# Kernel tuning notes

Hardware: AMD Instinct MI355X
Metric: run time of the kernel (lower is better)

The kernel has to match this reference:

```python
import jax, jax.numpy as jnp
import numpy as np

C = 256
CR = 32  # C // nc_reduce

def setup_inputs() -> dict:
    key = jax.random.key(0)
    ks = jax.random.split(key, 8)
    B, H, W = 4, 64, 64
    x = jax.random.normal(ks[0], (B, C, H, W), dtype=jnp.float32)
    s_in = 1.0 / np.sqrt(C)
    Wq = jax.random.uniform(ks[1], (CR, C), jnp.float32, -s_in, s_in)
    bq = jax.random.uniform(ks[2], (CR,), jnp.float32, -s_in, s_in)
    Wk = jax.random.uniform(ks[3], (CR, C), jnp.float32, -s_in, s_in)
    bk = jax.random.uniform(ks[4], (CR,), jnp.float32, -s_in, s_in)
    Wv = jax.random.uniform(ks[5], (C, C), jnp.float32, -s_in, s_in)
    bv = jax.random.uniform(ks[6], (C,), jnp.float32, -s_in, s_in)
    gamma = jnp.zeros((1,), dtype=jnp.float32)
    return {"x": x, "Wq": Wq, "bq": bq, "Wk": Wk, "bk": bk,
            "Wv": Wv, "bv": bv, "gamma": gamma}

def reference(x, Wq, bq, Wk, bk, Wv, bv, gamma):
    B, Cc, H, W = x.shape
    N = H * W
    xf = x.reshape(B, Cc, N)                       # [B, C, N]
    # 1x1 convs == per-position channel projections
    q = jnp.einsum('dc,bcn->bdn', Wq, xf) + bq[None, :, None]  # [B, CR, N]
    k = jnp.einsum('dc,bcn->bdn', Wk, xf) + bk[None, :, None]  # [B, CR, N]
    v = jnp.einsum('dc,bcn->bdn', Wv, xf) + bv[None, :, None]  # [B, C, N]
    # energy[b,i,j] = q[:, :, i] . k[:, :, j]  (no scaling, as in source)
    energy = jnp.einsum('bdi,bdj->bij', q, k)      # [B, N, N]
    attn = jax.nn.softmax(energy, axis=-1)
    # out[b,c,i] = sum_j v[b,c,j] * attn[b,i,j]
    outv = jnp.einsum('bcj,bij->bci', v, attn)     # [B, C, N]
    out = gamma[0] * outv.reshape(B, Cc, H, W) + x
    return out
```

## Files before the change

### kernel.cpp

```cpp
#include <hip/hip_runtime.h>
#include <hip/hip_bf16.h>

#define NB 4
#define CCH 256
#define CRD 32
#define NN 4096

typedef __attribute__((ext_vector_type(8))) short short8;
typedef __attribute__((ext_vector_type(4))) float floatx4;
typedef __attribute__((ext_vector_type(4))) int intx4;
typedef __attribute__((ext_vector_type(2))) unsigned int uintx2;

__device__ __forceinline__ unsigned short f2bf(float f) {
  unsigned u = __builtin_bit_cast(unsigned, f);
  u += 0x7FFFu + ((u >> 16) & 1u);
  return (unsigned short)(u >> 16);
}

__device__ __forceinline__ unsigned short f2bf_c(float f) {
  f = fminf(fmaxf(f, -1.0e4f), 1.0e4f);
  unsigned u = __builtin_bit_cast(unsigned, f);
  u += 0x7FFFu + ((u >> 16) & 1u);
  return (unsigned short)(u >> 16);
}

__device__ __forceinline__ unsigned pack2c(float a, float b) {
  return (unsigned)f2bf_c(a) | ((unsigned)f2bf_c(b) << 16);
}

__device__ __forceinline__ float sat(float v) {
  return fminf(fmaxf(v, -1.0e30f), 1.0e30f);
}

__device__ __forceinline__ short8 ld_frag_g(const unsigned short* p) {
  return __builtin_bit_cast(short8, *(const intx4*)p);
}

__global__ __launch_bounds__(256) void gemm_qkv_fused(
    const float* __restrict__ x,
    const float* __restrict__ Wq, const float* __restrict__ bq,
    const float* __restrict__ Wk, const float* __restrict__ bk,
    const float* __restrict__ Wv, const float* __restrict__ bv,
    unsigned short* __restrict__ qT, unsigned short* __restrict__ kT,
    unsigned short* __restrict__ vv)
{
  __shared__ __align__(16) unsigned short xs[64 * 264];
  __shared__ __align__(16) unsigned short ws[64 * 264];

  const int tid  = threadIdx.x;
  const int wave = tid >> 6;
  const int lane = tid & 63;
  const int lq   = lane >> 4;
  const int lm   = lane & 15;
  const int n0   = blockIdx.x << 6;
  const int mg   = blockIdx.y;
  const int b    = blockIdx.z;

  {
    const int nn = lane;
    const int cg = wave;
    const float* xb = x + ((size_t)b << 20) + n0 + nn;
#pragma unroll
    for (int it = 0; it < 16; ++it) {
      const int c0 = it * 16 + cg * 4;
      const float v0 = xb[(size_t)(c0 + 0) << 12];
      const float v1 = xb[(size_t)(c0 + 1) << 12];
      const float v2 = xb[(size_t)(c0 + 2) << 12];
      const float v3 = xb[(size_t)(c0 + 3) << 12];
      uintx2 u;
      u[0] = pack2c(v0, v1);
      u[1] = pack2c(v2, v3);
      *(uintx2*)(xs + nn * 264 + c0) = u;
    }
  }

  const int mt_lo = mg ? 3 : 0;
  const int mt_hi = mg ? 5 : 3;

  for (int mt = mt_lo; mt < mt_hi; ++mt) {
#pragma unroll
    for (int i = 0; i < 16; ++i) {
      const int u  = i * 256 + tid;
      const int m  = u >> 6;
      const int o4 = (u & 63) * 4;
      const float* src = (mt == 0)
          ? (m < 32 ? Wq + (size_t)m * CCH : Wk + (size_t)(m - 32) * CCH)
          : Wv + (size_t)((mt - 1) * 64 + m) * CCH;
      const floatx4 f = *(const floatx4*)(src + o4);
      uintx2 uu;
      uu[0] = pack2c(f[0], f[1]);
      uu[1] = pack2c(f[2], f[3]);
      *(uintx2*)(ws + m * 264 + o4) = uu;
    }
    __syncthreads();

    floatx4 acc[4];
#pragma unroll
    for (int t = 0; t < 4; ++t) acc[t] = (floatx4){0.f, 0.f, 0.f, 0.f};

#pragma unroll
    for (int k0 = 0; k0 < 8; ++k0) {
      short8 af[4];
#pragma unroll
      for (int ms = 0; ms < 4; ++ms)
        af[ms] = __builtin_bit_cast(short8,
            *(const intx4*)(ws + (ms * 16 + lm) * 264 + k0 * 32 + lq * 8));
      const short8 bf = __builtin_bit_cast(short8,
          *(const intx4*)(xs + (wave * 16 + lm) * 264 + k0 * 32 + lq * 8));
#pragma unroll
      for (int ms = 0; ms < 4; ++ms)
        acc[ms] = __builtin_amdgcn_mfma_f32_16x16x32_bf16(af[ms], bf,
                                                          acc[ms], 0, 0, 0);
    }
    __syncthreads();

    if (mt == 0) {
      const int n = n0 + wave * 16 + lm;
#pragma unroll
      for (int ms = 0; ms < 4; ++ms) {
        const int d0 = (ms & 1) * 16 + lq * 4;
        const float* bias = (ms < 2) ? bq : bk;
        unsigned short* dst = (ms < 2) ? qT : kT;
        uintx2 u;
        u[0] = pack2c(acc[ms][0] + bias[d0],     acc[ms][1] + bias[d0 + 1]);
        u[1] = pack2c(acc[ms][2] + bias[d0 + 2], acc[ms][3] + bias[d0 + 3]);
        *(uintx2*)(dst + (size_t)(b * NN + n) * CRD + d0) = u;
      }
    } else {
      const int cb = (mt - 1) * 64;
      unsigned short* vb2 = ws;
#pragma unroll
      for (int ms = 0; ms < 4; ++ms)
#pragma unroll
        for (int r = 0; r < 4; ++r) {
          const int c = ms * 16 + lq * 4 + r;
          vb2[c * 64 + wave * 16 + lm] = f2bf_c(acc[ms][r] + bv[cb + c]);
        }
      __syncthreads();
#pragma unroll
      for (int it = 0; it < 2; ++it) {
        const int u = it * 256 + tid;
        const int m = u >> 3;
        const int o = (u & 7) * 8;
        *(intx4*)(vv + (size_t)(b * CCH + cb + m) * NN + n0 + o) =
            *(const intx4*)(vb2 + m * 64 + o);
      }
      __syncthreads();
    }
  }
}

__global__ __launch_bounds__(512) void attn_kernel(
    const float* __restrict__ x, const float* __restrict__ gamma_p,
    const unsigned short* __restrict__ qT, const unsigned short* __restrict__ kT,
    const unsigned short* __restrict__ vv, float* __restrict__ out)
{
  __shared__ __align__(16) unsigned char smem[65536 + 2 * 4 * 2176];

  const int tid  = threadIdx.x;
  const int wave = tid >> 6;
  const int wg   = wave >> 1;
  const int cs   = wave & 1;
  const int lane = tid & 63;
  const int lq   = lane >> 4;
  const int lm   = lane & 15;
  const int xcd = blockIdx.x & 7;
  const int pos = blockIdx.x >> 3;
  const int b   = xcd >> 1;
  const int i0  = (((xcd & 1) << 5) | pos) << 6;

  const unsigned short* kTb = kT + (size_t)b * NN * CRD;
  const unsigned short* vb  = vv + (size_t)b * CCH * NN;

  const short8 qf =
      ld_frag_g(qT + (size_t)(b * NN + i0 + wg * 16 + lm) * CRD + lq * 8);

  int vs_g[4];
  int vs_off[4];
#pragma unroll
  for (int m = 0; m < 4; ++m) {
    const int u  = m * 512 + tid;
    const int c  = u >> 3;
    const int jb = u & 7;
    vs_g[m]   = c * NN + jb * 8;
    vs_off[m] = c * 128 + ((jb ^ (c & 7)) * 16);
  }

  floatx4 acc[8];
#pragma unroll
  for (int t = 0; t < 8; ++t) acc[t] = (floatx4){0.f, 0.f, 0.f, 0.f};
  float lsum[4] = {0.f, 0.f, 0.f, 0.f};

  intx4 vreg[4];
#pragma unroll
  for (int m = 0; m < 4; ++m)
    vreg[m] = *(const intx4*)(vb + vs_g[m]);
  short8 kf[2];
#pragma unroll
  for (int jt = 0; jt < 2; ++jt)
    kf[jt] = ld_frag_g(kTb + (size_t)((cs * 2 + jt) * 16 + lm) * CRD + lq * 8);

  const floatx4 zf = {0.f, 0.f, 0.f, 0.f};

#pragma unroll 1
  for (int k = 0; k < 64; ++k) {
    unsigned char* vbuf = smem + ((k & 1) << 15);
    unsigned char* pb   = smem + 65536 + (k & 1) * 8704 + wg * 2176;

#pragma unroll
    for (int m = 0; m < 4; ++m)
      *(intx4*)(vbuf + vs_off[m]) = vreg[m];

    floatx4 S[2];
#pragma unroll
    for (int jt = 0; jt < 2; ++jt) {
      S[jt] = __builtin_amdgcn_mfma_f32_16x16x32_bf16(qf, kf[jt], zf, 0, 0, 0);
#pragma unroll
      for (int r = 0; r < 4; ++r) {
        const float p = __expf(fminf(fmaxf(S[jt][r], -40.f), 40.f));
        S[jt][r] = p;
        lsum[r] += p;
      }
    }
#pragma unroll
    for (int jt = 0; jt < 2; ++jt)
#pragma unroll
      for (int r = 0; r < 4; ++r)
        *(unsigned short*)(pb + (lq * 4 + r) * 136 +
                           (((cs * 2 + jt) * 16 + lm) << 1)) = f2bf(S[jt][r]);

    asm volatile("s_waitcnt lgkmcnt(0)" ::: "memory");
    __builtin_amdgcn_s_barrier();

    if (k < 63) {
      const int j0n = (k + 1) << 6;
#pragma unroll
      for (int m = 0; m < 4; ++m)
        vreg[m] = *(const intx4*)(vb + vs_g[m] + j0n);
#pragma unroll
      for (int jt = 0; jt < 2; ++jt)
        kf[jt] = ld_frag_g(kTb +
                           (size_t)(j0n + (cs * 2 + jt) * 16 + lm) * CRD + lq * 8);
    }

#pragma unroll
    for (int ks = 0; ks < 2; ++ks) {
      const unsigned char* pa = pb + lm * 136 + ks * 64 + lq * 16;
      struct U128 { unsigned long long a, b; } pp;
      pp.a = *(const unsigned long long*)pa;
      pp.b = *(const unsigned long long*)(pa + 8);
      const short8 pf = __builtin_bit_cast(short8, pp);
#pragma unroll
      for (int nt = 0; nt < 8; ++nt) {
        const int c = cs * 128 + nt * 16 + lm;
        const short8 vf = __builtin_bit_cast(
            short8,
            *(const intx4*)(smem + ((k & 1) << 15) + c * 128 +
                            (((ks * 4 + lq) ^ (lm & 7)) * 16)));
        acc[nt] = __builtin_amdgcn_mfma_f32_16x16x32_bf16(pf, vf, acc[nt], 0, 0, 0);
      }
    }
    (void)vbuf;
  }

  __syncthreads();
  floatx4 lv;
#pragma unroll
  for (int r = 0; r < 4; ++r) lv[r] = lsum[r];
  *(floatx4*)(smem + ((wave * 64 + lane) << 4)) = lv;
  __syncthreads();
  const floatx4 lpart = *(const floatx4*)(smem + (((wave ^ 1) * 64 + lane) << 4));

  float inv[4];
#pragma unroll
  for (int r = 0; r < 4; ++r) {
    float v = lsum[r] + lpart[r];
    v += __shfl_xor(v, 1);
    v += __shfl_xor(v, 2);
    v += __shfl_xor(v, 4);
    v += __shfl_xor(v, 8);
    inv[r] = 1.0f / v;
  }

  const float gm = gamma_p[0];
#pragma unroll
  for (int nt = 0; nt < 8; ++nt) {
#pragma unroll
    for (int r = 0; r < 4; ++r) {
      const int c = cs * 128 + nt * 16 + lm;
      const int i = i0 + wg * 16 + lq * 4 + r;
      const size_t idx = (size_t)(b * CCH + c) * NN + i;
      out[idx] = gm * sat(acc[nt][r] * inv[r]) + x[idx];
    }
  }
}

extern "C" void kernel_launch(void* const* d_in, const int* in_sizes, int n_in,
                              void* d_out, int out_size, void* d_ws, size_t ws_size,
                              hipStream_t stream) {
  (void)in_sizes; (void)n_in; (void)out_size; (void)ws_size;
  const float* x     = (const float*)d_in[0];
  const float* Wq    = (const float*)d_in[1];
  const float* bq    = (const float*)d_in[2];
  const float* Wk    = (const float*)d_in[3];
  const float* bk    = (const float*)d_in[4];
  const float* Wv    = (const float*)d_in[5];
  const float* bv    = (const float*)d_in[6];
  const float* gamma = (const float*)d_in[7];

  unsigned short* qT = (unsigned short*)d_ws;
  unsigned short* kT = qT + (size_t)NB * NN * CRD;
  unsigned short* vv = kT + (size_t)NB * NN * CRD;

  gemm_qkv_fused<<<dim3(64, 2, 4), 256, 0, stream>>>(x, Wq, bq, Wk, bk, Wv, bv,
                                                     qT, kT, vv);
  attn_kernel<<<dim3(256, 1, 1), 512, 0, stream>>>(x, gamma, qT, kT, vv,
                                                   (float*)d_out);
}
```

Baseline: 166.3 us.

## Software-pipeline attention loop so next tile's scores overlap current PV MFMAs

```diff
diff --git a/kernel.cpp b/kernel.cpp
--- a/kernel.cpp
+++ b/kernel.cpp
@@ -191,6 +191,8 @@
   for (int t = 0; t < 8; ++t) acc[t] = (floatx4){0.f, 0.f, 0.f, 0.f};
   float lsum[4] = {0.f, 0.f, 0.f, 0.f};
 
+  const floatx4 zf = {0.f, 0.f, 0.f, 0.f};
+
   intx4 vreg[4];
 #pragma unroll
   for (int m = 0; m < 4; ++m)
@@ -200,52 +202,73 @@
   for (int jt = 0; jt < 2; ++jt)
     kf[jt] = ld_frag_g(kTb + (size_t)((cs * 2 + jt) * 16 + lm) * CRD + lq * 8);
 
-  const floatx4 zf = {0.f, 0.f, 0.f, 0.f};
+#pragma unroll
+  for (int m = 0; m < 4; ++m)
+    *(intx4*)(smem + vs_off[m]) = vreg[m];
+  {
+    unsigned char* pb0 = smem + 65536 + wg * 2176;
+#pragma unroll
+    for (int jt = 0; jt < 2; ++jt) {
+      const floatx4 S = __builtin_amdgcn_mfma_f32_16x16x32_bf16(
+          qf, kf[jt], zf, 0, 0, 0);
+#pragma unroll
+      for (int r = 0; r < 4; ++r) {
+        const float p = __expf(fminf(fmaxf(S[r], -40.f), 40.f));
+        lsum[r] += p;
+        *(unsigned short*)(pb0 + (lq * 4 + r) * 136 +
+                           (((cs * 2 + jt) * 16 + lm) << 1)) = f2bf(p);
+      }
+    }
+  }
+#pragma unroll
+  for (int m = 0; m < 4; ++m)
+    vreg[m] = *(const intx4*)(vb + vs_g[m] + 64);
+#pragma unroll
+  for (int jt = 0; jt < 2; ++jt)
+    kf[jt] = ld_frag_g(kTb + (size_t)(64 + (cs * 2 + jt) * 16 + lm) * CRD +
+                       lq * 8);
 
 #pragma unroll 1
-  for (int k = 0; k < 64; ++k) {
-    unsigned char* vbuf = smem + ((k & 1) << 15);
-    unsigned char* pb   = smem + 65536 + (k & 1) * 8704 + wg * 2176;
-
-#pragma unroll
-    for (int m = 0; m < 4; ++m)
-      *(intx4*)(vbuf + vs_off[m]) = vreg[m];
-
-    floatx4 S[2];
-#pragma unroll
-    for (int jt = 0; jt < 2; ++jt) {
-      S[jt] = __builtin_amdgcn_mfma_f32_16x16x32_bf16(qf, kf[jt], zf, 0, 0, 0);
-#pragma unroll
-      for (int r = 0; r < 4; ++r) {
-        const float p = __expf(fminf(fmaxf(S[jt][r], -40.f), 40.f));
-        S[jt][r] = p;
-        lsum[r] += p;
-      }
-    }
-#pragma unroll
-    for (int jt = 0; jt < 2; ++jt)
-#pragma unroll
-      for (int r = 0; r < 4; ++r)
-        *(unsigned short*)(pb + (lq * 4 + r) * 136 +
-                           (((cs * 2 + jt) * 16 + lm) << 1)) = f2bf(S[jt][r]);
-
+  for (int k = 0; k < 63; ++k) {
     asm volatile("s_waitcnt lgkmcnt(0)" ::: "memory");
     __builtin_amdgcn_s_barrier();
 
-    if (k < 63) {
-      const int j0n = (k + 1) << 6;
+    unsigned char* vbp = smem + ((k & 1) << 15);
+    unsigned char* pbp = smem + 65536 + (k & 1) * 8704 + wg * 2176;
+    unsigned char* vbn = smem + (((k + 1) & 1) << 15);
+    unsigned char* pbn = smem + 65536 + ((k + 1) & 1) * 8704 + wg * 2176;
+
+#pragma unroll
+    for (int m = 0; m < 4; ++m)
+      *(intx4*)(vbn + vs_off[m]) = vreg[m];
+
+#pragma unroll
+    for (int jt = 0; jt < 2; ++jt) {
+      const floatx4 S = __builtin_amdgcn_mfma_f32_16x16x32_bf16(
+          qf, kf[jt], zf, 0, 0, 0);
+#pragma unroll
+      for (int r = 0; r < 4; ++r) {
+        const float p = __expf(fminf(fmaxf(S[r], -40.f), 40.f));
+        lsum[r] += p;
+        *(unsigned short*)(pbn + (lq * 4 + r) * 136 +
+                           (((cs * 2 + jt) * 16 + lm) << 1)) = f2bf(p);
+      }
+    }
+
+    {
+      const int j2 = ((k + 2 < 64) ? (k + 2) : 63) << 6;
 #pragma unroll
       for (int m = 0; m < 4; ++m)
-        vreg[m] = *(const intx4*)(vb + vs_g[m] + j0n);
+        vreg[m] = *(const intx4*)(vb + vs_g[m] + j2);
 #pragma unroll
       for (int jt = 0; jt < 2; ++jt)
         kf[jt] = ld_frag_g(kTb +
-                           (size_t)(j0n + (cs * 2 + jt) * 16 + lm) * CRD + lq * 8);
+                           (size_t)(j2 + (cs * 2 + jt) * 16 + lm) * CRD + lq * 8);
     }
 
 #pragma unroll
     for (int ks = 0; ks < 2; ++ks) {
-      const unsigned char* pa = pb + lm * 136 + ks * 64 + lq * 16;
+      const unsigned char* pa = pbp + lm * 136 + ks * 64 + lq * 16;
       struct U128 { unsigned long long a, b; } pp;
       pp.a = *(const unsigned long long*)pa;
       pp.b = *(const unsigned long long*)(pa + 8);
@@ -255,12 +278,35 @@
         const int c = cs * 128 + nt * 16 + lm;
         const short8 vf = __builtin_bit_cast(
             short8,
-            *(const intx4*)(smem + ((k & 1) << 15) + c * 128 +
-                            (((ks * 4 + lq) ^ (lm & 7)) * 16)));
-        acc[nt] = __builtin_amdgcn_mfma_f32_16x16x32_bf16(pf, vf, acc[nt], 0, 0, 0);
-      }
-    }
-    (void)vbuf;
+            *(const intx4*)(vbp + c * 128 + (((ks * 4 + lq) ^ (lm & 7)) * 16)));
+        acc[nt] = __builtin_amdgcn_mfma_f32_16x16x32_bf16(pf, vf, acc[nt],
+                                                          0, 0, 0);
+      }
+    }
+  }
+
+  asm volatile("s_waitcnt lgkmcnt(0)" ::: "memory");
+  __builtin_amdgcn_s_barrier();
+  {
+    const unsigned char* vbp = smem + (1 << 15);
+    const unsigned char* pbp = smem + 65536 + 8704 + wg * 2176;
+#pragma unroll
+    for (int ks = 0; ks < 2; ++ks) {
+      const unsigned char* pa = pbp + lm * 136 + ks * 64 + lq * 16;
+      struct U128 { unsigned long long a, b; } pp;
+      pp.a = *(const unsigned long long*)pa;
+      pp.b = *(const unsigned long long*)(pa + 8);
+      const short8 pf = __builtin_bit_cast(short8, pp);
+#pragma unroll
+      for (int nt = 0; nt < 8; ++nt) {
+        const int c = cs * 128 + nt * 16 + lm;
+        const short8 vf = __builtin_bit_cast(
+            short8,
+            *(const intx4*)(vbp + c * 128 + (((ks * 4 + lq) ^ (lm & 7)) * 16)));
+        acc[nt] = __builtin_amdgcn_mfma_f32_16x16x32_bf16(pf, vf, acc[nt],
+                                                          0, 0, 0);
+      }
+    }
   }
 
   __syncthreads();
```

After: 159.6 us. -4.0%, faster.
